# Kernel optimization log

Hardware: AMD Instinct MI355X
Metric: run time of the kernel (lower is better)

## Reference

```python
import jax, jax.numpy as jnp
import numpy as np

D_MODEL, D_K, D_V, H = 1024, 64, 64, 16
B, NQ, NK = 2, 2048, 2048


def setup_inputs() -> dict:
    key = jax.random.key(0)
    ks = jax.random.split(key, 12)
    s = 0.02
    return {
        "queries": jax.random.normal(ks[0], (B, NQ, D_MODEL), jnp.float32),
        "keys": jax.random.normal(ks[1], (B, NK, D_MODEL), jnp.float32),
        "values": jax.random.normal(ks[2], (B, NK, D_MODEL), jnp.float32),
        "attention_weights": jax.random.uniform(ks[3], (B, H, NQ, NK), jnp.float32),
        "Wq": jax.random.normal(ks[4], (D_MODEL, H * D_K), jnp.float32) * s,
        "bq": jnp.zeros((H * D_K,), jnp.float32),
        "Wk": jax.random.normal(ks[5], (D_MODEL, H * D_K), jnp.float32) * s,
        "bk": jnp.zeros((H * D_K,), jnp.float32),
        "Wv": jax.random.normal(ks[6], (D_MODEL, H * D_V), jnp.float32) * s,
        "bv": jnp.zeros((H * D_V,), jnp.float32),
        "Wo": jax.random.normal(ks[7], (H * D_V, D_MODEL), jnp.float32) * s,
        "bo": jnp.zeros((D_MODEL,), jnp.float32),
    }


def reference(queries, keys, values, attention_weights, Wq, bq, Wk, bk, Wv, bv, Wo, bo):
    b_s, nq, _ = queries.shape
    nk = keys.shape[1]
    # projections -> (b, h, n, d)
    q = (queries @ Wq + bq).reshape(b_s, nq, H, D_K).transpose(0, 2, 1, 3)
    k = (keys @ Wk + bk).reshape(b_s, nk, H, D_K).transpose(0, 2, 1, 3)
    v = (values @ Wv + bv).reshape(b_s, nk, H, D_V).transpose(0, 2, 1, 3)
    # scaled scores, multiplicative weights, softmax (no mask; eval dropout = identity)
    att = jnp.einsum("bhqd,bhkd->bhqk", q, k) / jnp.sqrt(jnp.float32(D_K))
    att = att * attention_weights
    att = jax.nn.softmax(att, axis=-1)
    out = jnp.einsum("bhqk,bhkd->bhqd", att, v)
    out = out.transpose(0, 2, 1, 3).reshape(b_s, nq, H * D_V)
    return out @ Wo + bo
```

## Files before the change

kernel.cpp:

```cpp
#include <hip/hip_runtime.h>
#include <hip/hip_bf16.h>
#include <cstdint>
#include <cstddef>

typedef float f32x16 __attribute__((ext_vector_type(16)));
typedef float f32x4  __attribute__((ext_vector_type(4)));
typedef float f32x2  __attribute__((ext_vector_type(2)));
typedef float f32x4v __attribute__((ext_vector_type(4)));
typedef short short8 __attribute__((ext_vector_type(8)));
typedef unsigned short us4 __attribute__((ext_vector_type(4)));
typedef unsigned int u32;
typedef unsigned short u16;

#define MFMA32(a,b,c) __builtin_amdgcn_mfma_f32_32x32x16_bf16(a,b,c,0,0,0)
#define MFMA16(a,b,c) __builtin_amdgcn_mfma_f32_16x16x32_bf16(a,b,c,0,0,0)

#define HN 16
#define NQL 2048
#define NKL 2048
#define DM 1024

#define QSCALE 0.18033688011112042f

static __device__ __forceinline__ u16 f2bf(float f){
  union{float f;u32 u;}x; x.f=f; u32 u=x.u;
  return (u16)((u + 0x7fffu + ((u>>16)&1u))>>16);
}

#define AS1q __attribute__((address_space(1)))
#define AS3q __attribute__((address_space(3)))
static __device__ __forceinline__ void gload16(const void* g, void* l){
  __builtin_amdgcn_global_load_lds((const AS1q u32*)g, (AS3q u32*)l, 16, 0, 0);
}
static __device__ __forceinline__ void gload16nt(const void* g, void* l){
  __builtin_amdgcn_global_load_lds((const AS1q u32*)g, (AS3q u32*)l, 16, 0, 2);
}

#define OFF_ABF   (size_t)(0)
#define OFF_BTQKV (size_t)(25165824)
#define OFF_BTO   (size_t)(31457280)
#define OFF_QP    (size_t)(33554432)
#define OFF_KP    (size_t)(41943040)
#define OFF_VT    (size_t)(58720256)
#define OFF_AOUT  (size_t)(67108864)

__global__ void cast3_kernel(const float* __restrict__ q, const float* __restrict__ k,
                             const float* __restrict__ v, u16* __restrict__ dst){
  int i = blockIdx.x*256 + threadIdx.x;
  const float* src = (i < 1048576) ? q : (i < 2097152 ? k : v);
  int j = i & 1048575;
  f32x4v val = __builtin_nontemporal_load((const f32x4v*)src + j);
  ushort4 o; o.x=f2bf(val.x); o.y=f2bf(val.y); o.z=f2bf(val.z); o.w=f2bf(val.w);
  ((ushort4*)dst)[i] = o;
}

__global__ void twcast_kernel(const float* __restrict__ wq, const float* __restrict__ wk,
                              const float* __restrict__ wv, const float* __restrict__ wo,
                              u16* __restrict__ btqkv, u16* __restrict__ bto){
  __shared__ float tile[32][33];
  int which = blockIdx.z;
  const float* src = which==0?wq:which==1?wk:which==2?wv:wo;
  u16* dst = which<3 ? btqkv + (size_t)which*1024*1024 : bto;
  int n0 = blockIdx.x*32, k0 = blockIdx.y*32;
  int tx = threadIdx.x, ty = threadIdx.y;
  #pragma unroll
  for (int j=0;j<4;j++)
    tile[ty+8*j][tx] = __builtin_nontemporal_load(&src[(size_t)(k0+ty+8*j)*1024 + n0+tx]);
  __syncthreads();
  #pragma unroll
  for (int j=0;j<4;j++) dst[(size_t)(n0+ty+8*j)*1024 + k0+tx] = f2bf(tile[tx][ty+8*j]);
}

__global__ __launch_bounds__(256) void gemm0_kernel(
    const u16* __restrict__ Abase, const u16* __restrict__ Bt,
    const float* __restrict__ b0, const float* __restrict__ b1, const float* __restrict__ b2,
    u16* __restrict__ qp, u16* __restrict__ kp, u16* __restrict__ vt)
{
  __shared__ u16 lds[2*128*64];
  const int t = threadIdx.x;
  const int lane = t & 63, w = t >> 6;
  const int l15 = lane & 15, l4 = lane >> 4;
  const int n0 = blockIdx.x*128, m0 = blockIdx.y*128;
  const int which = n0 >> 10;
  const u16* A = Abase + (size_t)which*4096*1024;
  const int wr = w >> 1, wc = w & 1;

  f32x4 acc[4][4];
  #pragma unroll
  for (int i=0;i<4;i++)
    #pragma unroll
    for (int j=0;j<4;j++){ acc[i][j][0]=0.f; acc[i][j][1]=0.f; acc[i][j][2]=0.f; acc[i][j][3]=0.f; }

  for (int kk=0; kk<16; kk++){
    #pragma unroll
    for (int i=0;i<4;i++){
      int o = i*4096 + w*1024 + lane*16;
      int row = o >> 7, c16 = (o >> 4) & 7;
      int c16s = c16 ^ (row & 7);
      gload16(A + ((size_t)(m0+row)*1024 + kk*64 + c16s*8), (char*)lds + (i*4096 + w*1024));
    }
    #pragma unroll
    for (int i=0;i<4;i++){
      int o = i*4096 + w*1024 + lane*16;
      int row = o >> 7, c16 = (o >> 4) & 7;
      int c16s = c16 ^ (row & 7);
      gload16(Bt + ((size_t)(n0+row)*1024 + kk*64 + c16s*8), (char*)lds + 16384 + (i*4096 + w*1024));
    }
    __syncthreads();

    short8 af[4][2], bf[4][2];
    #pragma unroll
    for (int mr=0;mr<4;mr++)
      #pragma unroll
      for (int ks=0;ks<2;ks++){
        int row = wr*64 + mr*16 + l15;
        int c16 = ks*4 + l4;
        af[mr][ks] = *(const short8*)((const char*)lds + row*128 + ((c16 ^ (row&7))*16));
      }
    #pragma unroll
    for (int nc=0;nc<4;nc++)
      #pragma unroll
      for (int ks=0;ks<2;ks++){
        int row = wc*64 + nc*16 + l15;
        int c16 = ks*4 + l4;
        bf[nc][ks] = *(const short8*)((const char*)lds + 16384 + row*128 + ((c16 ^ (row&7))*16));
      }
    #pragma unroll
    for (int ks=0;ks<2;ks++)
      #pragma unroll
      for (int mr=0;mr<4;mr++)
        #pragma unroll
        for (int nc=0;nc<4;nc++)
          acc[mr][nc] = MFMA16(af[mr][ks], bf[nc][ks], acc[mr][nc]);
    __syncthreads();
  }

  if (which < 2){
    const float* bias = which==0?b0:b1;
    u16* dst = which==0?qp:kp;
    const float sc = (which==0) ? QSCALE : 1.0f;
    #pragma unroll
    for (int mr=0;mr<4;mr++)
      #pragma unroll
      for (int nc=0;nc<4;nc++)
        #pragma unroll
        for (int r=0;r<4;r++){
          int grow = m0 + wr*64 + mr*16 + l4*4 + r;
          int gcol = n0 + wc*64 + nc*16 + l15;
          int c1024 = gcol & 1023;
          float val = (acc[mr][nc][r] + bias[c1024]) * sc;
          int bsel = grow >> 11, nn = grow & 2047;
          int hh = c1024 >> 6, dd = gcol & 63;
          dst[((size_t)(bsel*HN+hh)*NQL + nn)*64 + dd] = f2bf(val);
        }
  } else {
    #pragma unroll
    for (int mr=0;mr<4;mr++)
      #pragma unroll
      for (int nc=0;nc<4;nc++){
        int grow0 = m0 + wr*64 + mr*16 + l4*4;
        int gcol = n0 + wc*64 + nc*16 + l15;
        int c1024 = gcol & 1023;
        int bsel = grow0 >> 11, nn = grow0 & 2047;
        int hh = c1024 >> 6, dd = c1024 & 63;
        float bv_ = b2[c1024];
        us4 pk;
        pk.x = f2bf(acc[mr][nc][0] + bv_);
        pk.y = f2bf(acc[mr][nc][1] + bv_);
        pk.z = f2bf(acc[mr][nc][2] + bv_);
        pk.w = f2bf(acc[mr][nc][3] + bv_);
        *(us4*)(vt + ((size_t)(bsel*HN+hh)*64 + dd)*NKL + nn) = pk;
      }
  }
}

__global__ __launch_bounds__(256) void gemm1_kernel(
    const u16* __restrict__ A, const u16* __restrict__ Bt,
    const float* __restrict__ bo, float* __restrict__ out)
{
  __shared__ u16 lds[(64+128)*64];
  const int t = threadIdx.x;
  const int lane = t & 63, w = t >> 6;
  const int l15 = lane & 15, l4 = lane >> 4;
  const int n0 = blockIdx.x*128, m0 = blockIdx.y*64;
  const int wr = w >> 1, wc = w & 1;

  f32x4 acc[2][4];
  #pragma unroll
  for (int i=0;i<2;i++)
    #pragma unroll
    for (int j=0;j<4;j++){ acc[i][j][0]=0.f; acc[i][j][1]=0.f; acc[i][j][2]=0.f; acc[i][j][3]=0.f; }

  for (int kk=0; kk<16; kk++){
    #pragma unroll
    for (int i=0;i<2;i++){
      int o = i*4096 + w*1024 + lane*16;
      int row = o >> 7, c16 = (o >> 4) & 7;
      int c16s = c16 ^ (row & 7);
      gload16(A + ((size_t)(m0+row)*1024 + kk*64 + c16s*8), (char*)lds + (i*4096 + w*1024));
    }
    #pragma unroll
    for (int i=0;i<4;i++){
      int o = i*4096 + w*1024 + lane*16;
      int row = o >> 7, c16 = (o >> 4) & 7;
      int c16s = c16 ^ (row & 7);
      gload16(Bt + ((size_t)(n0+row)*1024 + kk*64 + c16s*8), (char*)lds + 8192 + (i*4096 + w*1024));
    }
    __syncthreads();

    short8 af[2][2], bf[4][2];
    #pragma unroll
    for (int mr=0;mr<2;mr++)
      #pragma unroll
      for (int ks=0;ks<2;ks++){
        int row = wr*32 + mr*16 + l15;
        int c16 = ks*4 + l4;
        af[mr][ks] = *(const short8*)((const char*)lds + row*128 + ((c16 ^ (row&7))*16));
      }
    #pragma unroll
    for (int nc=0;nc<4;nc++)
      #pragma unroll
      for (int ks=0;ks<2;ks++){
        int row = wc*64 + nc*16 + l15;
        int c16 = ks*4 + l4;
        bf[nc][ks] = *(const short8*)((const char*)lds + 8192 + row*128 + ((c16 ^ (row&7))*16));
      }
    #pragma unroll
    for (int ks=0;ks<2;ks++)
      #pragma unroll
      for (int mr=0;mr<2;mr++)
        #pragma unroll
        for (int nc=0;nc<4;nc++)
          acc[mr][nc] = MFMA16(af[mr][ks], bf[nc][ks], acc[mr][nc]);
    __syncthreads();
  }

  #pragma unroll
  for (int mr=0;mr<2;mr++)
    #pragma unroll
    for (int nc=0;nc<4;nc++)
      #pragma unroll
      for (int r=0;r<4;r++){
        int grow = m0 + wr*32 + mr*16 + l4*4 + r;
        int gcol = n0 + wc*64 + nc*16 + l15;
        out[(size_t)grow*1024 + gcol] = acc[mr][nc][r] + bo[gcol];
      }
}

__global__ __launch_bounds__(512) void attn_kernel(
  const u16* __restrict__ qp, const u16* __restrict__ kp, const u16* __restrict__ vt,
  const float* __restrict__ wts, u16* __restrict__ aout)
{
  __shared__ __align__(16) char lds[131072];
  char* kl = lds;
  char* vl = lds + 16384;
  const int tid = threadIdx.x;
  const int lane = tid & 63, wid = tid >> 6;
  const int lo = lane & 31, hi = lane >> 5;
  char* wl = lds + 32768 + wid*8192;
  char* pl = lds + 98304 + wid*4096;

  const int g = blockIdx.x;
  const int j = g >> 3;
  const int bh = (g & 7)*4 + (j >> 3);
  const int qblk = j & 7;
  const int b = bh >> 4;
  const int q0 = qblk*256 + wid*32;

  const u16* qb = qp + ((size_t)bh*NQL + q0)*64;
  const u16* kb = kp + (size_t)bh*NKL*64;
  const u16* vb = vt + (size_t)bh*64*NKL;
  const float* wb = wts + ((size_t)bh*NQL + q0)*(size_t)NKL;

  short8 qf[4];
  #pragma unroll
  for (int ks=0;ks<4;ks++)
    qf[ks] = *(const short8*)(qb + (size_t)lo*64 + ks*16 + hi*8);

  f32x16 o0, o1;
  float ls[16];
  #pragma unroll
  for (int r=0;r<16;r++){ o0[r]=0.f; o1[r]=0.f; ls[r]=0.f; }

  const int krow = tid >> 3, ksl = tid & 7;
  const int le16 = lane & 15, ld16 = lane >> 4;

  {
    gload16(kb + (size_t)krow*64 + (ksl ^ ((krow>>1)&7))*8, kl + tid*16);
    gload16(vb + (size_t)krow*NKL + (ksl ^ (krow&7))*8,     vl + tid*16);
    #pragma unroll
    for (int i=0;i<8;i++){
      int q = 4*i + ld16;
      gload16nt(wb + (size_t)q*NKL + le16*4, wl + i*1024);
    }
  }
  __syncthreads();

  for (int kt=0; kt<32; kt++){
    const int cur = (kt&1)*8192;
    const int nxt = cur ^ 8192;
    const int kb0 = kt*64;

    if (kt < 31){
      int kb1 = kb0 + 64;
      gload16(kb + (size_t)(kb1+krow)*64 + (ksl ^ ((krow>>1)&7))*8, kl + nxt + tid*16);
      gload16(vb + (size_t)krow*NKL + kb1 + (ksl ^ (krow&7))*8,     vl + nxt + tid*16);
    }

    f32x2 wp[16];
    #pragma unroll
    for (int r=0;r<16;r++){
      int qr = (r&3) + 8*(r>>2) + 4*hi;
      wp[r] = *(const f32x2*)(wl + qr*256 + lo*8);
    }
    short8 kf0[4], kf1[4];
    #pragma unroll
    for (int ks=0;ks<4;ks++){
      int slot = (ks*2 + hi) ^ (lo&7);
      kf0[ks] = *(const short8*)(kl + cur + (2*lo)*128 + slot*16);
      kf1[ks] = *(const short8*)(kl + cur + (2*lo)*128 + 128 + slot*16);
    }
    asm volatile("s_waitcnt lgkmcnt(0)" ::: "memory");
    __builtin_amdgcn_sched_barrier(0);

    if (kt < 31){
      int kb1 = kb0 + 64;
      #pragma unroll
      for (int i=0;i<8;i++){
        int q = 4*i + ld16;
        gload16nt(wb + (size_t)q*NKL + kb1 + le16*4, wl + i*1024);
      }
    }

    f32x16 s0, s1;
    #pragma unroll
    for (int r=0;r<16;r++){ s0[r]=0.f; s1[r]=0.f; }
    #pragma unroll
    for (int ks=0;ks<4;ks++){
      s0 = MFMA32(qf[ks], kf0[ks], s0);
      s1 = MFMA32(qf[ks], kf1[ks], s1);
    }

    short8 vf0[4], vf1[4];
    #pragma unroll
    for (int t=0;t<4;t++){
      int slot = (t*2 + hi) ^ (lo&7);
      vf0[t] = *(const short8*)(vl + cur + lo*128 + slot*16);
      vf1[t] = *(const short8*)(vl + cur + (32+lo)*128 + slot*16);
    }

    #pragma unroll
    for (int r=0;r<16;r++){
      float p0 = exp2f(s0[r] * wp[r].x);
      float p1 = exp2f(s1[r] * wp[r].y);
      ls[r] += p0 + p1;
      u32 pk;
      asm("v_cvt_pk_bf16_f32 %0, %1, %2" : "=v"(pk) : "v"(p0), "v"(p1));
      int row = (r&3) + 8*(r>>2) + 4*hi;
      *(u32*)(pl + row*128 + ((lo*4) ^ ((row&7)<<4))) = pk;
    }
    asm volatile("s_waitcnt lgkmcnt(0)" ::: "memory");
    short8 pf[4];
    #pragma unroll
    for (int t=0;t<4;t++)
      pf[t] = *(const short8*)(pl + lo*128 + ((t*32 + hi*16) ^ ((lo&7)<<4)));
    #pragma unroll
    for (int t=0;t<4;t++){
      o0 = MFMA32(pf[t], vf0[t], o0);
      o1 = MFMA32(pf[t], vf1[t], o1);
    }
    __syncthreads();
  }

  u16* ob = aout + ((size_t)b*NQL + q0)*DM + (bh & 15)*64;
  #pragma unroll
  for (int r=0;r<16;r++){
    float L = ls[r];
    L += __shfl_xor(L,1); L += __shfl_xor(L,2); L += __shfl_xor(L,4);
    L += __shfl_xor(L,8); L += __shfl_xor(L,16);
    float inv = 1.0f / L;
    int q = (r&3) + 8*(r>>2) + 4*hi;
    ob[(size_t)q*DM + lo]      = f2bf(o0[r]*inv);
    ob[(size_t)q*DM + 32 + lo] = f2bf(o1[r]*inv);
  }
}

extern "C" void kernel_launch(void* const* d_in, const int* in_sizes, int n_in,
                              void* d_out, int out_size, void* d_ws, size_t ws_size,
                              hipStream_t stream){
  const float* queries = (const float*)d_in[0];
  const float* keys    = (const float*)d_in[1];
  const float* values  = (const float*)d_in[2];
  const float* attw    = (const float*)d_in[3];
  const float* Wq = (const float*)d_in[4];
  const float* bq = (const float*)d_in[5];
  const float* Wk = (const float*)d_in[6];
  const float* bk = (const float*)d_in[7];
  const float* Wv = (const float*)d_in[8];
  const float* bv = (const float*)d_in[9];
  const float* Wo = (const float*)d_in[10];
  const float* bo = (const float*)d_in[11];
  char* ws = (char*)d_ws;
  u16* abf   = (u16*)(ws + OFF_ABF);
  u16* btqkv = (u16*)(ws + OFF_BTQKV);
  u16* bto   = (u16*)(ws + OFF_BTO);
  u16* qp    = (u16*)(ws + OFF_QP);
  u16* kp    = (u16*)(ws + OFF_KP);
  u16* vt    = (u16*)(ws + OFF_VT);
  u16* aout  = (u16*)(ws + OFF_AOUT);
  float* out = (float*)d_out;

  cast3_kernel<<<12288, 256, 0, stream>>>(queries, keys, values, abf);
  twcast_kernel<<<dim3(32,32,4), dim3(32,8), 0, stream>>>(Wq,Wk,Wv,Wo,btqkv,bto);
  gemm0_kernel<<<dim3(24,32), 256, 0, stream>>>(abf, btqkv, bq,bk,bv, qp,kp,vt);
  attn_kernel<<<256, 512, 0, stream>>>(qp, kp, vt, attw, aout);
  gemm1_kernel<<<dim3(8,64), 256, 0, stream>>>(aout, bto, bo, out);
}
```

Before: 213.5 us.

## Load attention weights directly to registers and swizzle GEMM block order

```diff
diff --git a/kernel.cpp b/kernel.cpp
--- a/kernel.cpp
+++ b/kernel.cpp
@@ -31,9 +31,6 @@
 #define AS3q __attribute__((address_space(3)))
 static __device__ __forceinline__ void gload16(const void* g, void* l){
   __builtin_amdgcn_global_load_lds((const AS1q u32*)g, (AS3q u32*)l, 16, 0, 0);
-}
-static __device__ __forceinline__ void gload16nt(const void* g, void* l){
-  __builtin_amdgcn_global_load_lds((const AS1q u32*)g, (AS3q u32*)l, 16, 0, 2);
 }
 
 #define OFF_ABF   (size_t)(0)
@@ -80,7 +77,9 @@
   const int t = threadIdx.x;
   const int lane = t & 63, w = t >> 6;
   const int l15 = lane & 15, l4 = lane >> 4;
-  const int n0 = blockIdx.x*128, m0 = blockIdx.y*128;
+  const int lin = blockIdx.y*24 + blockIdx.x;
+  const int swz = (lin & 7)*96 + (lin >> 3);
+  const int n0 = (swz % 24)*128, m0 = (swz / 24)*128;
   const int which = n0 >> 10;
   const u16* A = Abase + (size_t)which*4096*1024;
   const int wr = w >> 1, wc = w & 1;
@@ -182,7 +181,9 @@
   const int t = threadIdx.x;
   const int lane = t & 63, w = t >> 6;
   const int l15 = lane & 15, l4 = lane >> 4;
-  const int n0 = blockIdx.x*128, m0 = blockIdx.y*64;
+  const int lin = blockIdx.y*8 + blockIdx.x;
+  const int swz = (lin & 7)*64 + (lin >> 3);
+  const int n0 = (swz & 7)*128, m0 = (swz >> 3)*64;
   const int wr = w >> 1, wc = w & 1;
 
   f32x4 acc[2][4];
@@ -251,14 +252,13 @@
   const u16* __restrict__ qp, const u16* __restrict__ kp, const u16* __restrict__ vt,
   const float* __restrict__ wts, u16* __restrict__ aout)
 {
-  __shared__ __align__(16) char lds[131072];
+  __shared__ __align__(16) char lds[65536];
   char* kl = lds;
   char* vl = lds + 16384;
   const int tid = threadIdx.x;
   const int lane = tid & 63, wid = tid >> 6;
   const int lo = lane & 31, hi = lane >> 5;
-  char* wl = lds + 32768 + wid*8192;
-  char* pl = lds + 98304 + wid*4096;
+  char* pl = lds + 32768 + wid*4096;
 
   const int g = blockIdx.x;
   const int j = g >> 3;
@@ -283,54 +283,49 @@
   for (int r=0;r<16;r++){ o0[r]=0.f; o1[r]=0.f; ls[r]=0.f; }
 
   const int krow = tid >> 3, ksl = tid & 7;
-  const int le16 = lane & 15, ld16 = lane >> 4;
+
+  float wx[2][16], wy[2][16];
 
   {
     gload16(kb + (size_t)krow*64 + (ksl ^ ((krow>>1)&7))*8, kl + tid*16);
     gload16(vb + (size_t)krow*NKL + (ksl ^ (krow&7))*8,     vl + tid*16);
     #pragma unroll
-    for (int i=0;i<8;i++){
-      int q = 4*i + ld16;
-      gload16nt(wb + (size_t)q*NKL + le16*4, wl + i*1024);
+    for (int r=0;r<16;r++){
+      int qr = (r&3) + 8*(r>>2) + 4*hi;
+      f32x2 wv = __builtin_nontemporal_load((const f32x2*)(wb + (size_t)qr*NKL) + lo);
+      wx[0][r] = wv.x; wy[0][r] = wv.y;
     }
   }
   __syncthreads();
 
+  #pragma unroll 2
   for (int kt=0; kt<32; kt++){
-    const int cur = (kt&1)*8192;
-    const int nxt = cur ^ 8192;
+    const int curb = (kt&1)*8192;
+    const int nxtb = curb ^ 8192;
+    const int cur = kt & 1;
     const int kb0 = kt*64;
 
     if (kt < 31){
       int kb1 = kb0 + 64;
-      gload16(kb + (size_t)(kb1+krow)*64 + (ksl ^ ((krow>>1)&7))*8, kl + nxt + tid*16);
-      gload16(vb + (size_t)krow*NKL + kb1 + (ksl ^ (krow&7))*8,     vl + nxt + tid*16);
-    }
-
-    f32x2 wp[16];
-    #pragma unroll
-    for (int r=0;r<16;r++){
-      int qr = (r&3) + 8*(r>>2) + 4*hi;
-      wp[r] = *(const f32x2*)(wl + qr*256 + lo*8);
-    }
+      gload16(kb + (size_t)(kb1+krow)*64 + (ksl ^ ((krow>>1)&7))*8, kl + nxtb + tid*16);
+      gload16(vb + (size_t)krow*NKL + kb1 + (ksl ^ (krow&7))*8,     vl + nxtb + tid*16);
+      #pragma unroll
+      for (int r=0;r<16;r++){
+        int qr = (r&3) + 8*(r>>2) + 4*hi;
+        f32x2 wv = __builtin_nontemporal_load((const f32x2*)(wb + (size_t)qr*NKL + kb1) + lo);
+        wx[cur^1][r] = wv.x; wy[cur^1][r] = wv.y;
+      }
+    }
+
     short8 kf0[4], kf1[4];
     #pragma unroll
     for (int ks=0;ks<4;ks++){
       int slot = (ks*2 + hi) ^ (lo&7);
-      kf0[ks] = *(const short8*)(kl + cur + (2*lo)*128 + slot*16);
-      kf1[ks] = *(const short8*)(kl + cur + (2*lo)*128 + 128 + slot*16);
+      kf0[ks] = *(const short8*)(kl + curb + (2*lo)*128 + slot*16);
+      kf1[ks] = *(const short8*)(kl + curb + (2*lo)*128 + 128 + slot*16);
     }
     asm volatile("s_waitcnt lgkmcnt(0)" ::: "memory");
     __builtin_amdgcn_sched_barrier(0);
-
-    if (kt < 31){
-      int kb1 = kb0 + 64;
-      #pragma unroll
-      for (int i=0;i<8;i++){
-        int q = 4*i + ld16;
-        gload16nt(wb + (size_t)q*NKL + kb1 + le16*4, wl + i*1024);
-      }
-    }
 
     f32x16 s0, s1;
     #pragma unroll
@@ -345,14 +340,14 @@
     #pragma unroll
     for (int t=0;t<4;t++){
       int slot = (t*2 + hi) ^ (lo&7);
-      vf0[t] = *(const short8*)(vl + cur + lo*128 + slot*16);
-      vf1[t] = *(const short8*)(vl + cur + (32+lo)*128 + slot*16);
+      vf0[t] = *(const short8*)(vl + curb + lo*128 + slot*16);
+      vf1[t] = *(const short8*)(vl + curb + (32+lo)*128 + slot*16);
     }
 
     #pragma unroll
     for (int r=0;r<16;r++){
-      float p0 = exp2f(s0[r] * wp[r].x);
-      float p1 = exp2f(s1[r] * wp[r].y);
+      float p0 = exp2f(s0[r] * wx[cur][r]);
+      float p1 = exp2f(s1[r] * wy[cur][r]);
       ls[r] += p0 + p1;
       u32 pk;
       asm("v_cvt_pk_bf16_f32 %0, %1, %2" : "=v"(pk) : "v"(p0), "v"(p1));
```

After: 219.6 us. 1.03x slower.
